# Kernel tuning notes

Measured on AMD Instinct MI355X. Metric: run time of the kernel, lower is better.

The kernel has to match this reference:

```python
import jax, jax.numpy as jnp
import numpy as np

D_MODEL = 256
B, H, T = 4, 8, 2048
EPS = 1e-8


def _clinear(x_r, x_i, w_r, w_i, b_r, b_i):
    # complex matmul: (x_r + i x_i) @ (w_r + i w_i)^T + (b_r + i b_i)
    y_r = jnp.matmul(x_r, w_r.T) - jnp.matmul(x_i, w_i.T) + b_r
    y_i = jnp.matmul(x_i, w_r.T) + jnp.matmul(x_r, w_i.T) + b_i
    return y_r, y_i


def setup_inputs() -> dict:
    key = jax.random.key(0)
    ks = jax.random.split(key, 24)
    d = D_MODEL
    std = np.sqrt(2.0 / (d + d)) / np.sqrt(2.0)  # glorot-ish * 1/sqrt(2) as in _init_weights
    inp = {}
    inp['q_in_r'] = jax.random.normal(ks[0], (B, H, T, d), jnp.float32)
    inp['q_in_i'] = jax.random.normal(ks[1], (B, H, T, d), jnp.float32)
    inp['kv_in_r'] = jax.random.normal(ks[2], (B, H, T, d), jnp.float32)
    inp['kv_in_i'] = jax.random.normal(ks[3], (B, H, T, d), jnp.float32)
    i = 4
    for p in ['q', 'k', 'v', 'o']:
        inp[p + '_wr'] = std * jax.random.normal(ks[i], (d, d), jnp.float32); i += 1
        inp[p + '_wi'] = std * jax.random.normal(ks[i], (d, d), jnp.float32); i += 1
        inp[p + '_br'] = jnp.zeros((d,), jnp.float32)
        inp[p + '_bi'] = jnp.zeros((d,), jnp.float32)
    inp['gate_w'] = std * jax.random.normal(ks[i], (d, d), jnp.float32)
    inp['gate_b'] = jnp.zeros((d,), jnp.float32)
    return inp


def reference(q_in_r, q_in_i, kv_in_r, kv_in_i,
              q_wr, q_wi, q_br, q_bi,
              k_wr, k_wi, k_br, k_bi,
              v_wr, v_wi, v_br, v_bi,
              o_wr, o_wi, o_br, o_bi,
              gate_w, gate_b):
    D = q_in_r.shape[-1]
    q_r, q_i = _clinear(q_in_r, q_in_i, q_wr, q_wi, q_br, q_bi)
    k_r, k_i = _clinear(kv_in_r, kv_in_i, k_wr, k_wi, k_br, k_bi)
    v_r, v_i = _clinear(kv_in_r, kv_in_i, v_wr, v_wi, v_br, v_bi)
    scale = 1.0 / np.sqrt(D)
    # real part of complex inner product <q, k> (the module's dual-part score)
    scores = (jnp.einsum('bhqd,bhkd->bhqk', q_r, k_r)
              + jnp.einsum('bhqd,bhkd->bhqk', q_i, k_i)) * scale
    attn = jax.nn.softmax(scores, axis=-1)
    ctx_r = jnp.einsum('bhqk,bhkd->bhqd', attn, v_r)
    ctx_i = jnp.einsum('bhqk,bhkd->bhqd', attn, v_i)
    out_r, out_i = _clinear(ctx_r, ctx_i, o_wr, o_wi, o_br, o_bi)
    out_mag = jnp.sqrt(out_r ** 2 + out_i ** 2 + EPS)
    gate = jax.nn.sigmoid(jnp.matmul(out_mag, gate_w.T) + gate_b)
    return out_r * gate, out_i * gate
```

## Files before the change

kernel.cpp:

```cpp
#include <hip/hip_runtime.h>
#include <hip/hip_bf16.h>
#include <hip/hip_fp16.h>
#include <stdint.h>


#define TSEQ   2048
#define NHEADS 32
#define MTOT   65536
#define DDC    512
#define HCHUNK 8

typedef float    f32x4  __attribute__((ext_vector_type(4)));
typedef _Float16 f16x8  __attribute__((ext_vector_type(8)));
typedef uint16_t u16x4  __attribute__((ext_vector_type(4)));
typedef uint16_t u16x8  __attribute__((ext_vector_type(8)));

__device__ __forceinline__ uint16_t f2h(float f) {
  _Float16 h = (_Float16)f;
  return __builtin_bit_cast(uint16_t, h);
}
__device__ __forceinline__ float h2f(uint16_t u) {
  return (float)__builtin_bit_cast(_Float16, u);
}

__device__ __forceinline__ void gld16(const void* g, void* l) {
  __builtin_amdgcn_global_load_lds(
      (const __attribute__((address_space(1))) uint32_t*)g,
      (__attribute__((address_space(3))) uint32_t*)l, 16, 0, 0);
}

enum { EP_F16Z = 0, EP_PROJ = 1, EP_OUT = 2, EP_GATE = 3 };

template <int EP, int BM>
__global__ __launch_bounds__(512, 2) void gemm_bt(
    const uint16_t* __restrict__ A, int lda, long zA,
    const uint16_t* __restrict__ B, int ldb, long zB,
    void* __restrict__ C, int ldc, long zC, int K,
    const float* __restrict__ biasR, const float* __restrict__ biasI,
    float scale, float* __restrict__ outR, float* __restrict__ outI) {
  constexpr int MI    = BM / 32;
  constexpr int ASLAB = BM / 64;
  constexpr int ABUFE = BM * 64;
  constexpr int BUFE  = (BM + 256) * 64;
  __shared__ uint16_t lds[2 * BUFE];

  const int tid  = threadIdx.x;
  const int wave = tid >> 6;
  const int lane = tid & 63;
  const int wr   = (wave >> 2) * (BM / 2);
  const int wc   = (wave & 3) * 64;

  const int gx = gridDim.x, gy = gridDim.y;
  const int nwg = gx * gy * gridDim.z;
  const int lin = blockIdx.x + gx * (blockIdx.y + gy * blockIdx.z);
  const int cpx = nwg >> 3;
  const int swz = (lin & 7) * cpx + (lin >> 3);
  const int shx = __popc(gx - 1);
  const int shy = __popc(gy - 1);
  const int bx = swz & (gx - 1);
  const int by = (swz >> shx) & (gy - 1);
  const int bz = swz >> (shx + shy);

  const long tm = (long)by * BM;
  const long tn = (long)bx * 256;
  const uint16_t* Ab = A + (long)bz * zA;
  const uint16_t* Bb = B + (long)bz * zB;

  f32x4 acc[MI][4] = {};

  const int arow   = wave * 8 + (lane >> 3);
  const int schunk = (lane & 7) ^ (lane >> 3);

  const int fr   = lane & 15;
  const int quad = lane >> 4;
  const int sw   = fr & 7;
  const int ch0  = ((0 + quad) ^ sw) * 16;
  const int ch1  = ((4 + quad) ^ sw) * 16;

  const int nt = K >> 6;

  auto STAGE = [&](int buf, int t) {
    const long k0 = (long)t * 64 + schunk * 8;
    uint16_t* base = lds + buf * BUFE;
#pragma unroll
    for (int s = 0; s < ASLAB; ++s)
      gld16(Ab + (tm + s * 64 + arow) * (long)lda + k0,
            base + (s * 64 + wave * 8) * 64);
#pragma unroll
    for (int s = 0; s < 4; ++s)
      gld16(Bb + (tn + s * 64 + arow) * (long)ldb + k0,
            base + ABUFE + (s * 64 + wave * 8) * 64);
  };

  auto COMPUTE = [&](int buf) {
    const char* Abase = (const char*)(lds + buf * BUFE);
    const char* Bbase = Abase + 2 * ABUFE;
#pragma unroll
    for (int ks = 0; ks < 2; ++ks) {
      const int co = ks ? ch1 : ch0;
      f16x8 bf[4];
#pragma unroll
      for (int j = 0; j < 4; ++j)
        bf[j] = *(const f16x8*)(Bbase + (wc + j * 16 + fr) * 128 + co);
#pragma unroll
      for (int i = 0; i < MI; ++i) {
        const f16x8 af = *(const f16x8*)(Abase + (wr + i * 16 + fr) * 128 + co);
#pragma unroll
        for (int j = 0; j < 4; ++j)
          acc[i][j] = __builtin_amdgcn_mfma_f32_16x16x32_f16(af, bf[j], acc[i][j], 0, 0, 0);
      }
    }
  };

  STAGE(0, 0);
  __syncthreads();
  int cur = 0;
  for (int t = 0; t + 1 < nt; ++t) {
    STAGE(cur ^ 1, t + 1);
    COMPUTE(cur);
    __syncthreads();
    cur ^= 1;
  }
  COMPUTE(cur);

  if constexpr (EP == EP_F16Z || EP == EP_PROJ) {
    __syncthreads();
    char* wbase = (char*)lds + wave * (BM * 64);
    uint16_t* Cp = (uint16_t*)C + ((EP == EP_F16Z) ? (long)bz * zC : 0L);
#pragma unroll
    for (int i = 0; i < MI; ++i) {
#pragma unroll
      for (int j = 0; j < 4; ++j) {
#pragma unroll
        for (int r = 0; r < 4; ++r) {
          const int row = i * 16 + quad * 4 + r;
          int byte = row * 128 + (j * 16 + fr) * 2;
          byte ^= ((row >> 2) & 3) << 5;
          float v = acc[i][j][r];
          if constexpr (EP == EP_PROJ) {
            const int col = (int)tn + wc + j * 16 + fr;
            v += (col < 256) ? biasR[col] : biasI[col - 256];
          } else {
            v *= scale;
          }
          *(uint16_t*)(wbase + byte) = f2h(v);
        }
      }
    }
    asm volatile("s_waitcnt lgkmcnt(0)" ::: "memory");
    __builtin_amdgcn_sched_barrier(0);
#pragma unroll
    for (int it = 0; it < BM / 16; ++it) {
      const int row = it * 8 + (lane >> 3);
      const int c   = lane & 7;
      int byte = row * 128 + c * 16;
      byte ^= ((row >> 2) & 3) << 5;
      const u16x8 val = *(const u16x8*)(wbase + byte);
      const long grow = tm + wr + row;
      const int  gcol = (int)tn + wc + c * 8;
      *(u16x8*)(Cp + grow * (long)ldc + gcol) = val;
    }
  } else {
#pragma unroll
    for (int i = 0; i < MI; ++i) {
      const long row0 = tm + wr + i * 16 + quad * 4;
#pragma unroll
      for (int j = 0; j < 4; ++j) {
        const int col = (int)tn + wc + j * 16 + fr;
#pragma unroll
        for (int r = 0; r < 4; ++r) {
          float v = acc[i][j][r];
          const long rw = row0 + r;
          if constexpr (EP == EP_OUT) {
            if (col < 256) outR[rw * 256 + col]       = v + biasR[col];
            else           outI[rw * 256 + col - 256] = v + biasI[col - 256];
          } else {
            const float g = 1.0f / (1.0f + __expf(-(v + biasR[col])));
            const long o = rw * 256 + col;
            outR[o] *= g;
            outI[o] *= g;
          }
        }
      }
    }
  }
}

__global__ void pack_x(const float* __restrict__ xr, const float* __restrict__ xi,
                       uint16_t* __restrict__ out) {
  const long idx = (long)blockIdx.x * 256 + threadIdx.x;
  const long m  = idx >> 7;
  const int  c4 = (int)(idx & 127) << 2;
  const float* src = (c4 < 256) ? (xr + m * 256 + c4) : (xi + m * 256 + (c4 - 256));
  const float4 v = *(const float4*)src;
  u16x4 o = {f2h(v.x), f2h(v.y), f2h(v.z), f2h(v.w)};
  *(u16x4*)(out + m * 512 + c4) = o;
}

__global__ void pack_w(const float* __restrict__ wr, const float* __restrict__ wi,
                       uint16_t* __restrict__ out) {
  const int idx = blockIdx.x * 256 + threadIdx.x;
  const int j  = idx >> 7;
  const int c4 = (idx & 127) << 2;
  const float* src;
  float sgn = 1.f;
  if (j < 256) {
    if (c4 < 256) src = wr + j * 256 + c4;
    else { src = wi + j * 256 + (c4 - 256); sgn = -1.f; }
  } else {
    if (c4 < 256) src = wi + (j - 256) * 256 + c4;
    else          src = wr + (j - 256) * 256 + (c4 - 256);
  }
  const float4 v = *(const float4*)src;
  u16x4 o = {f2h(sgn * v.x), f2h(sgn * v.y), f2h(sgn * v.z), f2h(sgn * v.w)};
  *(u16x4*)(out + (long)j * 512 + c4) = o;
}

__global__ void pack_gw(const float* __restrict__ w, uint16_t* __restrict__ out) {
  const int idx = blockIdx.x * 256 + threadIdx.x;
  const float4 v = *(const float4*)(w + (long)idx * 4);
  u16x4 o = {f2h(v.x), f2h(v.y), f2h(v.z), f2h(v.w)};
  *(u16x4*)(out + (long)idx * 4) = o;
}

__global__ void transpose_v(const uint16_t* __restrict__ V, uint16_t* __restrict__ Vt) {
  __shared__ uint16_t t[32][33];
  const int h = blockIdx.z;
  const uint16_t* Vh = V + (long)h * TSEQ * DDC;
  uint16_t* Vth = Vt + (long)h * DDC * TSEQ;
  const int t0 = blockIdx.x * 32;
  const int n0 = blockIdx.y * 32;
  const int lx = threadIdx.x & 31, ly = threadIdx.x >> 5;
#pragma unroll
  for (int yy = ly; yy < 32; yy += 8)
    t[yy][lx] = Vh[(long)(t0 + yy) * DDC + n0 + lx];
  __syncthreads();
#pragma unroll
  for (int yy = ly; yy < 32; yy += 8)
    Vth[(long)(n0 + yy) * TSEQ + t0 + lx] = t[lx][yy];
}

__global__ __launch_bounds__(256) void softmax_rows(uint16_t* __restrict__ S) {
  const long row = blockIdx.x;
  uint16_t* p = S + row * 2048;
  const int tid = threadIdx.x;
  u16x8 raw = ((const u16x8*)p)[tid];
  float v[8];
#pragma unroll
  for (int j = 0; j < 8; ++j) v[j] = h2f(raw[j]);
  float m = v[0];
#pragma unroll
  for (int j = 1; j < 8; ++j) m = fmaxf(m, v[j]);
#pragma unroll
  for (int off = 32; off >= 1; off >>= 1) m = fmaxf(m, __shfl_xor(m, off));
  __shared__ float red[8];
  const int wave = tid >> 6, lane = tid & 63;
  if (lane == 0) red[wave] = m;
  __syncthreads();
  m = fmaxf(fmaxf(red[0], red[1]), fmaxf(red[2], red[3]));
  float s = 0.f;
#pragma unroll
  for (int j = 0; j < 8; ++j) { v[j] = __expf(v[j] - m); s += v[j]; }
#pragma unroll
  for (int off = 32; off >= 1; off >>= 1) s += __shfl_xor(s, off);
  if (lane == 0) red[4 + wave] = s;
  __syncthreads();
  s = red[4] + red[5] + red[6] + red[7];
  const float inv = 1.0f / s;
  u16x8 o;
#pragma unroll
  for (int j = 0; j < 8; ++j) o[j] = f2h(v[j] * inv);
  ((u16x8*)p)[tid] = o;
}

__global__ void mag_kernel(const float* __restrict__ R, const float* __restrict__ I,
                           uint16_t* __restrict__ mag) {
  const long i = ((long)blockIdx.x * 256 + threadIdx.x) * 4;
  const float4 r  = *(const float4*)(R + i);
  const float4 im = *(const float4*)(I + i);
  u16x4 o = {f2h(sqrtf(r.x * r.x + im.x * im.x + 1e-8f)),
             f2h(sqrtf(r.y * r.y + im.y * im.y + 1e-8f)),
             f2h(sqrtf(r.z * r.z + im.z * im.z + 1e-8f)),
             f2h(sqrtf(r.w * r.w + im.w * im.w + 1e-8f))};
  *(u16x4*)(mag + i) = o;
}

extern "C" void kernel_launch(void* const* d_in, const int* in_sizes, int n_in,
                              void* d_out, int out_size, void* d_ws, size_t ws_size,
                              hipStream_t stream) {
  const float* q_in_r  = (const float*)d_in[0];
  const float* q_in_i  = (const float*)d_in[1];
  const float* kv_in_r = (const float*)d_in[2];
  const float* kv_in_i = (const float*)d_in[3];
  const float* q_wr = (const float*)d_in[4];
  const float* q_wi = (const float*)d_in[5];
  const float* q_br = (const float*)d_in[6];
  const float* q_bi = (const float*)d_in[7];
  const float* k_wr = (const float*)d_in[8];
  const float* k_wi = (const float*)d_in[9];
  const float* k_br = (const float*)d_in[10];
  const float* k_bi = (const float*)d_in[11];
  const float* v_wr = (const float*)d_in[12];
  const float* v_wi = (const float*)d_in[13];
  const float* v_br = (const float*)d_in[14];
  const float* v_bi = (const float*)d_in[15];
  const float* o_wr = (const float*)d_in[16];
  const float* o_wi = (const float*)d_in[17];
  const float* o_br = (const float*)d_in[18];
  const float* o_bi = (const float*)d_in[19];
  const float* gate_w = (const float*)d_in[20];
  const float* gate_b = (const float*)d_in[21];

  unsigned char* w = (unsigned char*)d_ws;
  const size_t MAT16 = (size_t)MTOT * DDC * 2;
  size_t off = 0;
  uint16_t* R1 = (uint16_t*)(w + off); off += MAT16;
  uint16_t* R2 = (uint16_t*)(w + off); off += MAT16;
  uint16_t* R3 = (uint16_t*)(w + off); off += MAT16;
  uint16_t* R4 = (uint16_t*)(w + off); off += MAT16;
  uint16_t* R5 = (uint16_t*)(w + off); off += MAT16;
  uint16_t* Wq = (uint16_t*)(w + off); off += 512 * 512 * 2;
  uint16_t* Wk = (uint16_t*)(w + off); off += 512 * 512 * 2;
  uint16_t* Wv = (uint16_t*)(w + off); off += 512 * 512 * 2;
  uint16_t* Wo = (uint16_t*)(w + off); off += 512 * 512 * 2;
  uint16_t* Gw = (uint16_t*)(w + off); off += 256 * 256 * 2;

  uint16_t* Xq  = R1; uint16_t* Vt  = R1;
  uint16_t* Xkv = R2; uint16_t* Ctx = R2;
  uint16_t* Qm  = R3; uint16_t* Mag = R3;
  uint16_t* Km  = R4;
  uint16_t* Vm  = R5; uint16_t* Sc  = R5;

  float* outR = (float*)d_out;
  float* outI = (float*)d_out + (long)MTOT * 256;

  pack_x<<<32768, 256, 0, stream>>>(q_in_r, q_in_i, Xq);
  pack_x<<<32768, 256, 0, stream>>>(kv_in_r, kv_in_i, Xkv);
  pack_w<<<256, 256, 0, stream>>>(q_wr, q_wi, Wq);
  pack_w<<<256, 256, 0, stream>>>(k_wr, k_wi, Wk);
  pack_w<<<256, 256, 0, stream>>>(v_wr, v_wi, Wv);
  pack_w<<<256, 256, 0, stream>>>(o_wr, o_wi, Wo);
  pack_gw<<<64, 256, 0, stream>>>(gate_w, Gw);

  gemm_bt<EP_PROJ, 256><<<dim3(2, 256, 1), 512, 0, stream>>>(
      Xq, 512, 0, Wq, 512, 0, Qm, 512, 0, 512, q_br, q_bi, 1.f, nullptr, nullptr);
  gemm_bt<EP_PROJ, 256><<<dim3(2, 256, 1), 512, 0, stream>>>(
      Xkv, 512, 0, Wk, 512, 0, Km, 512, 0, 512, k_br, k_bi, 1.f, nullptr, nullptr);
  gemm_bt<EP_PROJ, 256><<<dim3(2, 256, 1), 512, 0, stream>>>(
      Xkv, 512, 0, Wv, 512, 0, Vm, 512, 0, 512, v_br, v_bi, 1.f, nullptr, nullptr);
  transpose_v<<<dim3(64, 16, 32), 256, 0, stream>>>(Vm, Vt);

  for (int c = 0; c < NHEADS / HCHUNK; ++c) {
    const long ho = (long)c * HCHUNK;
    gemm_bt<EP_F16Z, 256><<<dim3(8, 8, HCHUNK), 512, 0, stream>>>(
        Qm + ho * TSEQ * DDC, 512, (long)TSEQ * DDC,
        Km + ho * TSEQ * DDC, 512, (long)TSEQ * DDC,
        Sc, TSEQ, (long)TSEQ * TSEQ, 512, nullptr, nullptr, 0.0625f, nullptr, nullptr);
    softmax_rows<<<HCHUNK * TSEQ, 256, 0, stream>>>(Sc);
    gemm_bt<EP_F16Z, 128><<<dim3(2, 16, HCHUNK), 512, 0, stream>>>(
        Sc, TSEQ, (long)TSEQ * TSEQ,
        Vt + ho * DDC * TSEQ, TSEQ, (long)DDC * TSEQ,
        Ctx + ho * TSEQ * DDC, 512, (long)TSEQ * DDC, 2048,
        nullptr, nullptr, 1.f, nullptr, nullptr);
  }

  gemm_bt<EP_OUT, 256><<<dim3(2, 256, 1), 512, 0, stream>>>(
      Ctx, 512, 0, Wo, 512, 0, nullptr, 0, 0, 512, o_br, o_bi, 1.f, outR, outI);

  mag_kernel<<<16384, 256, 0, stream>>>(outR, outI, Mag);

  gemm_bt<EP_GATE, 256><<<dim3(1, 256, 1), 512, 0, stream>>>(
      Mag, 256, 0, Gw, 256, 0, nullptr, 0, 0, 256, gate_b, nullptr, 1.f, outR, outI);
}
```

Measured before the change: 1.137 ms.

## Fuse K/V projections into one GEMM and relax main-loop barriers

The K and V projections become a single GEMM with twice the output columns, relying on Wk and Wv sitting next to each other in the workspace. The epilogue sends the upper half of the columns to the V buffer, and a small kernel pre-concatenates the biases, so the shared X_kv input is read only once. The main GEMM loop now waits with explicit vmcnt counts and raw s_barrier instead of full __syncthreads, so the prefetch of the next tile can stay in flight during compute. Launch bounds for BM=128 are raised to 4 waves per SIMD, which caps register use and risks spills.

```diff
diff --git a/kernel.cpp b/kernel.cpp
--- a/kernel.cpp
+++ b/kernel.cpp
@@ -32,16 +32,18 @@
 enum { EP_F16Z = 0, EP_PROJ = 1, EP_OUT = 2, EP_GATE = 3 };
 
 template <int EP, int BM>
-__global__ __launch_bounds__(512, 2) void gemm_bt(
+__global__ __launch_bounds__(512, (BM == 128) ? 4 : 2) void gemm_bt(
     const uint16_t* __restrict__ A, int lda, long zA,
     const uint16_t* __restrict__ B, int ldb, long zB,
-    void* __restrict__ C, int ldc, long zC, int K,
+    void* __restrict__ C, int ldc, long zC, uint16_t* __restrict__ CV,
+    int K,
     const float* __restrict__ biasR, const float* __restrict__ biasI,
     float scale, float* __restrict__ outR, float* __restrict__ outI) {
   constexpr int MI    = BM / 32;
   constexpr int ASLAB = BM / 64;
   constexpr int ABUFE = BM * 64;
   constexpr int BUFE  = (BM + 256) * 64;
+  constexpr int NLOAD = ASLAB + 4;
   __shared__ uint16_t lds[2 * BUFE];
 
   const int tid  = threadIdx.x;
@@ -113,20 +115,37 @@
   };
 
   STAGE(0, 0);
-  __syncthreads();
   int cur = 0;
-  for (int t = 0; t + 1 < nt; ++t) {
-    STAGE(cur ^ 1, t + 1);
+  for (int t = 0; t < nt; ++t) {
+    if (t + 1 < nt) {
+      STAGE(cur ^ 1, t + 1);
+      if constexpr (NLOAD == 8)      asm volatile("s_waitcnt vmcnt(8)" ::: "memory");
+      else if constexpr (NLOAD == 6) asm volatile("s_waitcnt vmcnt(6)" ::: "memory");
+      else                           asm volatile("s_waitcnt vmcnt(0)" ::: "memory");
+    } else {
+      asm volatile("s_waitcnt vmcnt(0)" ::: "memory");
+    }
+    __builtin_amdgcn_s_barrier();
+    __builtin_amdgcn_sched_barrier(0);
     COMPUTE(cur);
-    __syncthreads();
+    __builtin_amdgcn_sched_barrier(0);
+    __builtin_amdgcn_s_barrier();
+    __builtin_amdgcn_sched_barrier(0);
     cur ^= 1;
   }
-  COMPUTE(cur);
 
   if constexpr (EP == EP_F16Z || EP == EP_PROJ) {
     __syncthreads();
     char* wbase = (char*)lds + wave * (BM * 64);
-    uint16_t* Cp = (uint16_t*)C + ((EP == EP_F16Z) ? (long)bz * zC : 0L);
+    uint16_t* Cp;
+    int coff = 0;
+    if constexpr (EP == EP_PROJ) {
+      const bool vhalf = (CV != nullptr) && (tn >= 512);
+      Cp = vhalf ? CV : (uint16_t*)C;
+      coff = vhalf ? 512 : 0;
+    } else {
+      Cp = (uint16_t*)C + (long)bz * zC;
+    }
 #pragma unroll
     for (int i = 0; i < MI; ++i) {
 #pragma unroll
@@ -139,7 +158,7 @@
           float v = acc[i][j][r];
           if constexpr (EP == EP_PROJ) {
             const int col = (int)tn + wc + j * 16 + fr;
-            v += (col < 256) ? biasR[col] : biasI[col - 256];
+            v += biasR[col];
           } else {
             v *= scale;
           }
@@ -157,7 +176,7 @@
       byte ^= ((row >> 2) & 3) << 5;
       const u16x8 val = *(const u16x8*)(wbase + byte);
       const long grow = tm + wr + row;
-      const int  gcol = (int)tn + wc + c * 8;
+      const int  gcol = (int)tn + wc + c * 8 - coff;
       *(u16x8*)(Cp + grow * (long)ldc + gcol) = val;
     }
   } else {
@@ -221,6 +240,19 @@
   const float4 v = *(const float4*)(w + (long)idx * 4);
   u16x4 o = {f2h(v.x), f2h(v.y), f2h(v.z), f2h(v.w)};
   *(u16x4*)(out + (long)idx * 4) = o;
+}
+
+__global__ void pack_bias(const float* __restrict__ qbr, const float* __restrict__ qbi,
+                          const float* __restrict__ kbr, const float* __restrict__ kbi,
+                          const float* __restrict__ vbr, const float* __restrict__ vbi,
+                          float* __restrict__ bq, float* __restrict__ bkv) {
+  const int i = blockIdx.x * 256 + threadIdx.x;
+  if (i < 256)       bq[i] = qbr[i];
+  else if (i < 512)  bq[i] = qbi[i - 256];
+  else if (i < 768)  bkv[i - 512] = kbr[i - 512];
+  else if (i < 1024) bkv[i - 512] = kbi[i - 768];
+  else if (i < 1280) bkv[i - 512] = vbr[i - 1024];
+  else               bkv[i - 512] = vbi[i - 1280];
 }
 
 __global__ void transpose_v(const uint16_t* __restrict__ V, uint16_t* __restrict__ Vt) {
@@ -324,6 +356,8 @@
   uint16_t* Wv = (uint16_t*)(w + off); off += 512 * 512 * 2;
   uint16_t* Wo = (uint16_t*)(w + off); off += 512 * 512 * 2;
   uint16_t* Gw = (uint16_t*)(w + off); off += 256 * 256 * 2;
+  float*    Bq  = (float*)(w + off);   off += 512 * 4;
+  float*    Bkv = (float*)(w + off);   off += 1024 * 4;
 
   uint16_t* Xq  = R1; uint16_t* Vt  = R1;
   uint16_t* Xkv = R2; uint16_t* Ctx = R2;
@@ -341,13 +375,14 @@
   pack_w<<<256, 256, 0, stream>>>(v_wr, v_wi, Wv);
   pack_w<<<256, 256, 0, stream>>>(o_wr, o_wi, Wo);
   pack_gw<<<64, 256, 0, stream>>>(gate_w, Gw);
+  pack_bias<<<6, 256, 0, stream>>>(q_br, q_bi, k_br, k_bi, v_br, v_bi, Bq, Bkv);
 
   gemm_bt<EP_PROJ, 256><<<dim3(2, 256, 1), 512, 0, stream>>>(
-      Xq, 512, 0, Wq, 512, 0, Qm, 512, 0, 512, q_br, q_bi, 1.f, nullptr, nullptr);
-  gemm_bt<EP_PROJ, 256><<<dim3(2, 256, 1), 512, 0, stream>>>(
-      Xkv, 512, 0, Wk, 512, 0, Km, 512, 0, 512, k_br, k_bi, 1.f, nullptr, nullptr);
-  gemm_bt<EP_PROJ, 256><<<dim3(2, 256, 1), 512, 0, stream>>>(
-      Xkv, 512, 0, Wv, 512, 0, Vm, 512, 0, 512, v_br, v_bi, 1.f, nullptr, nullptr);
+      Xq, 512, 0, Wq, 512, 0, Qm, 512, 0, nullptr, 512, Bq, nullptr, 1.f,
+      nullptr, nullptr);
+  gemm_bt<EP_PROJ, 256><<<dim3(4, 256, 1), 512, 0, stream>>>(
+      Xkv, 512, 0, Wk, 512, 0, Km, 512, 0, Vm, 512, Bkv, nullptr, 1.f,
+      nullptr, nullptr);
   transpose_v<<<dim3(64, 16, 32), 256, 0, stream>>>(Vm, Vt);
 
   for (int c = 0; c < NHEADS / HCHUNK; ++c) {
@@ -355,20 +390,23 @@
     gemm_bt<EP_F16Z, 256><<<dim3(8, 8, HCHUNK), 512, 0, stream>>>(
         Qm + ho * TSEQ * DDC, 512, (long)TSEQ * DDC,
         Km + ho * TSEQ * DDC, 512, (long)TSEQ * DDC,
-        Sc, TSEQ, (long)TSEQ * TSEQ, 512, nullptr, nullptr, 0.0625f, nullptr, nullptr);
+        Sc, TSEQ, (long)TSEQ * TSEQ, nullptr, 512,
+        nullptr, nullptr, 0.0625f, nullptr, nullptr);
     softmax_rows<<<HCHUNK * TSEQ, 256, 0, stream>>>(Sc);
     gemm_bt<EP_F16Z, 128><<<dim3(2, 16, HCHUNK), 512, 0, stream>>>(
         Sc, TSEQ, (long)TSEQ * TSEQ,
         Vt + ho * DDC * TSEQ, TSEQ, (long)DDC * TSEQ,
-        Ctx + ho * TSEQ * DDC, 512, (long)TSEQ * DDC, 2048,
+        Ctx + ho * TSEQ * DDC, 512, (long)TSEQ * DDC, nullptr, 2048,
         nullptr, nullptr, 1.f, nullptr, nullptr);
   }
 
   gemm_bt<EP_OUT, 256><<<dim3(2, 256, 1), 512, 0, stream>>>(
-      Ctx, 512, 0, Wo, 512, 0, nullptr, 0, 0, 512, o_br, o_bi, 1.f, outR, outI);
+      Ctx, 512, 0, Wo, 512, 0, nullptr, 0, 0, nullptr, 512,
+      o_br, o_bi, 1.f, outR, outI);
 
   mag_kernel<<<16384, 256, 0, stream>>>(outR, outI, Mag);
 
   gemm_bt<EP_GATE, 256><<<dim3(1, 256, 1), 512, 0, stream>>>(
-      Mag, 256, 0, Gw, 256, 0, nullptr, 0, 0, 256, gate_b, nullptr, 1.f, outR, outI);
-}
+      Mag, 256, 0, Gw, 256, 0, nullptr, 0, 0, nullptr, 256,
+      gate_b, nullptr, 1.f, outR, outI);
+}
```

After: 1.119 ms. Within noise of the previous version (-1.6%).
